# Kernel tuning notes

Measured on AMD Instinct MI355X. Metric: run time of the kernel, lower is better.

Reference implementation:

```python
import jax, jax.numpy as jnp
import numpy as np
from math import sqrt

B = 128        # graphs
P = 256        # nodes per graph
N = B * P      # total nodes
E = 524288     # edges (avg degree 16)
S = 32         # seed queries per graph
DQ = DK = DV = 128
H = 4          # heads


def setup_inputs() -> dict:
    key = jax.random.key(0)
    ks = jax.random.split(key, 10)
    Q = jax.random.normal(ks[0], (B, S, DQ), dtype=jnp.float32)
    x = jax.random.normal(ks[1], (N, DK), dtype=jnp.float32)
    # edges constrained within each graph block of P nodes
    src = jax.random.randint(ks[2], (E,), 0, N)
    dst = (src // P) * P + jax.random.randint(ks[3], (E,), 0, P)
    edge_index = jnp.stack([src, dst]).astype(jnp.int64)
    batch = (jnp.arange(N) // P).astype(jnp.int64)
    s = 1.0 / sqrt(DV)
    Wq = jax.random.normal(ks[4], (DQ, DV), dtype=jnp.float32) * s
    Wk = jax.random.normal(ks[5], (DK, DV), dtype=jnp.float32) * s
    Wv = jax.random.normal(ks[6], (DK, DV), dtype=jnp.float32) * s
    Wo = jax.random.normal(ks[7], (DV, DV), dtype=jnp.float32) * s
    z = jnp.zeros((DV,), jnp.float32)
    o = jnp.ones((DV,), jnp.float32)
    return {"Q": Q, "x": x, "edge_index": edge_index, "batch": batch,
            "Wq": Wq, "bq": z, "Wk": Wk, "bk": z, "Wv": Wv, "bv": z,
            "Wo": Wo, "bo": z, "g0": o, "b0": z, "g1": o, "b1": z}


def _gcn(x, edge_index, W, b):
    # PyG GCNConv: self-loops + symmetric deg^-1/2 normalization, then scatter-add
    xw = x @ W                                   # [N, DV]
    row, col = edge_index[0], edge_index[1]
    deg = jnp.zeros((N,), xw.dtype).at[col].add(1.0) + 1.0  # +1 for self-loop
    dinv = jax.lax.rsqrt(deg)
    coef = dinv[row] * dinv[col]                 # [E]
    out = jnp.zeros_like(xw).at[col].add(xw[row] * coef[:, None])
    out = out + xw * (dinv * dinv)[:, None]      # self-loop messages
    return out + b


def _ln(x, g, b, eps=1e-5):
    mu = x.mean(-1, keepdims=True)
    var = ((x - mu) ** 2).mean(-1, keepdims=True)
    return (x - mu) * jax.lax.rsqrt(var + eps) * g + b


def reference(Q, x, edge_index, batch, Wq, bq, Wk, bk, Wv, bv, Wo, bo, g0, b0, g1, b1):
    dh = DV // H
    Qp = Q @ Wq + bq                             # [B, S, DV]
    K = _gcn(x, edge_index, Wk, bk)              # [N, DV]
    V = _gcn(x, edge_index, Wv, bv)
    # to_dense_batch: equal-size graphs -> static reshape; mask all valid
    Kd = K.reshape(B, P, DV)
    Vd = V.reshape(B, P, DV)
    mask = jnp.ones((B, P), Qp.dtype)
    mask_add = (1.0 - mask) * -1e9               # [B, P]
    # split heads on last dim (== torch split(dim=2) + cat(dim=0))
    Qh = Qp.reshape(B, S, H, dh)
    Kh = Kd.reshape(B, P, H, dh)
    Vh = Vd.reshape(B, P, H, dh)
    scores = jnp.einsum('bshd,bphd->bhsp', Qh, Kh) / sqrt(DV)
    A = jax.nn.softmax(scores + mask_add[:, None, None, :], axis=-1)
    Oh = Qh + jnp.einsum('bhsp,bphd->bshd', A, Vh)
    O = Oh.reshape(B, S, DV)
    O = _ln(O, g0, b0)
    O = O + jax.nn.relu(O @ Wo + bo)
    O = _ln(O, g1, b1)
    return O
```

## Files before the change

### kernel.cpp

```cpp
#include <hip/hip_runtime.h>

typedef unsigned int uint32;
typedef unsigned short ushort;
typedef __attribute__((ext_vector_type(8))) short short8;
typedef __attribute__((ext_vector_type(4))) float f32x4;

#define NNODES 32768
#define NGRAPH 128
#define PNODES 256
#define SQ 32
#define NEDGE 524288
#define DIM 128
#define NHEAD 4
#define MAXDEG 64

__device__ __forceinline__ float u2f(uint32 u){ union{uint32 i; float f;} c; c.i=u; return c.f; }
__device__ __forceinline__ uint32 f2bf(float f){
  union{float f; uint32 i;} c; c.f=f;
  return (c.i + 0x7FFFu + ((c.i>>16)&1u)) >> 16;
}
__device__ __forceinline__ uint32 pk2(float a, float b){ return f2bf(a) | (f2bf(b)<<16); }

__device__ __forceinline__ void swz_pair(int b, int& g, int& h){
  const int xcd = b & 7, j = b >> 3;
  g = xcd * 16 + (j >> 1);
  h = j & 1;
}

__global__ __launch_bounds__(256) void k_prep0(const float* __restrict__ Wk,
    const float* __restrict__ Wv, const float* __restrict__ Wq, const float* __restrict__ Wo,
    ushort* __restrict__ WTk, ushort* __restrict__ WTv, ushort* __restrict__ WTq,
    ushort* __restrict__ WTo, int4* __restrict__ zbase){
  const int bid = blockIdx.x;
  const int t = threadIdx.x;
  if (bid >= 4){
    int idx = (bid-4)*256 + t;
    if (idx < 8192) zbase[idx] = int4{0,0,0,0};
    return;
  }
  __shared__ __align__(16) float Ws2[128*132];
  const float* W = (bid==0) ? Wk : (bid==1) ? Wv : (bid==2) ? Wq : Wo;
  ushort* WT     = (bid==0) ? WTk : (bid==1) ? WTv : (bid==2) ? WTq : WTo;
  for (int idx = t; idx < 4096; idx += 256){
    int k = idx >> 5, c4 = idx & 31;
    *(float4*)&Ws2[k*132 + c4*4] = *(const float4*)&W[k*128 + c4*4];
  }
  __syncthreads();
  for (int idx = t; idx < 2048; idx += 256){
    int n = idx & 127, c8 = idx >> 7;
    uint4 p;
    p.x = pk2(Ws2[(c8*8+0)*132 + n], Ws2[(c8*8+1)*132 + n]);
    p.y = pk2(Ws2[(c8*8+2)*132 + n], Ws2[(c8*8+3)*132 + n]);
    p.z = pk2(Ws2[(c8*8+4)*132 + n], Ws2[(c8*8+5)*132 + n]);
    p.w = pk2(Ws2[(c8*8+6)*132 + n], Ws2[(c8*8+7)*132 + n]);
    *(uint4*)&WT[n*128 + c8*8] = p;
  }
}

__global__ void k_edges(const int* __restrict__ ei, int* __restrict__ deg,
                        ushort* __restrict__ ebuf){
  int e = blockIdx.x*256 + threadIdx.x;
  int s = ei[e];
  int d = ei[NEDGE + e];
  int i = atomicAdd(&deg[d], 1);
  if (i < MAXDEG) ebuf[(d << 6) + i] = (ushort)(s & 255);
}

#define APITCH 132
__global__ __launch_bounds__(512) void k_aggkv(
    const int* __restrict__ deg, const ushort* __restrict__ ebuf,
    const float* __restrict__ x,
    const ushort* __restrict__ WTk, const float* __restrict__ bk, ushort* __restrict__ Kb,
    const ushort* __restrict__ WTv, const float* __restrict__ bv, ushort* __restrict__ VbT)
{
  __shared__ __align__(16) char lds[138240];
  uint32* A    = (uint32*)lds;
  ushort* Au   = (ushort*)lds;
  ushort* xT   = (ushort*)(lds + 67584);
  ushort* xa_s = (ushort*)(lds + 67584);
  ushort* wtA  = (ushort*)(lds + 102400);
  ushort* wtB  = (ushort*)(lds + 0);
  ushort* KK   = (ushort*)(lds + 67584);
  ushort* VVt  = (ushort*)(lds + 102400);
  float*  dvs  = (float*)(lds + 137216);
  const int t = threadIdx.x;
  int g, half;
  swz_pair(blockIdx.x, g, half);
  const int base = g*PNODES;
  const int rbase = half*128;

  if (t < 256) dvs[t] = rsqrtf((float)(deg[base + t] + 1));
  {
    uint4* Az = (uint4*)A;
    for (int i = t; i < 4224; i += 512) Az[i] = uint4{0,0,0,0};
  }
  __syncthreads();
  if (t < 128){
    float dn = dvs[rbase + t];
    int src = rbase + t;
    uint32 nb = f2bf(dn*dn);
    A[t*APITCH + (src>>1)] = (src & 1) ? (nb<<16) : nb;
  }
  for (int idx = t; idx < 8192; idx += 512){
    int f = idx & 127, s4 = idx >> 7;
    const int r = base + s4*4;
    float v0 = x[(r+0)*DIM + f];
    float v1 = x[(r+1)*DIM + f];
    float v2 = x[(r+2)*DIM + f];
    float v3 = x[(r+3)*DIM + f];
    uint2 p; p.x = pk2(v0, v1); p.y = pk2(v2, v3);
    *(uint2*)&xT[f*264 + s4*4] = p;
  }
  __syncthreads();
  {
    const int r = t >> 2, sub = t & 3;
    const int n = base + rbase + r;
    const int dg = min(deg[n], MAXDEG);
    const float dn = dvs[rbase + r];
    const ushort* eb = ebuf + (n << 6);
    for (int i = 0; i < dg; ++i){
      const int srcl = eb[i];
      if (((srcl >> 1) & 3) != sub) continue;
      const float coef = dn * dvs[srcl];
      uint32* cell = &A[r*APITCH + (srcl>>1)];
      uint32 old = *cell;
      if (srcl & 1){
        float cur = u2f(old & 0xffff0000u);
        *cell = (old & 0xffffu) | (f2bf(cur + coef) << 16);
      } else {
        float cur = u2f(old << 16);
        *cell = (old & 0xffff0000u) | f2bf(cur + coef);
      }
    }
  }
  __syncthreads();
  const int lane = t & 63, w = t >> 6;
  const int r16 = lane & 15, kg = lane >> 4;
  f32x4 acc[8];
  #pragma unroll
  for (int j = 0; j < 8; ++j) acc[j] = (f32x4){0.f,0.f,0.f,0.f};
  #pragma unroll
  for (int kc = 0; kc < 8; ++kc){
    const short8 a = *(const short8*)&Au[(w*16 + r16)*264 + kc*32 + kg*8];
    #pragma unroll
    for (int ct = 0; ct < 8; ++ct){
      const short8 b = *(const short8*)&xT[(ct*16 + r16)*264 + kc*32 + kg*8];
      acc[ct] = __builtin_amdgcn_mfma_f32_16x16x32_bf16(a, b, acc[ct], 0, 0, 0);
    }
  }
  __syncthreads();
  #pragma unroll
  for (int ct = 0; ct < 8; ++ct)
    #pragma unroll
    for (int q = 0; q < 4; ++q)
      xa_s[(w*16 + kg*4 + q)*136 + ct*16 + r16] = (ushort)f2bf(acc[ct][q]);
  for (int idx = t; idx < 2048; idx += 512){
    int n = idx >> 4, c8 = idx & 15;
    *(uint4*)&wtA[n*136 + c8*8] = *(const uint4*)&WTk[n*128 + c8*8];
    *(uint4*)&wtB[n*136 + c8*8] = *(const uint4*)&WTv[n*128 + c8*8];
  }
  __syncthreads();
  f32x4 k0[8], v0[8];
  #pragma unroll
  for (int j = 0; j < 8; ++j){ k0[j] = (f32x4){0.f,0.f,0.f,0.f}; v0[j] = (f32x4){0.f,0.f,0.f,0.f}; }
  #pragma unroll
  for (int kc = 0; kc < 4; ++kc){
    const short8 a = *(const short8*)&xa_s[(w*16 + r16)*136 + kc*32 + kg*8];
    #pragma unroll
    for (int ct = 0; ct < 8; ++ct){
      const short8 b0 = *(const short8*)&wtA[(ct*16 + r16)*136 + kc*32 + kg*8];
      const short8 b1 = *(const short8*)&wtB[(ct*16 + r16)*136 + kc*32 + kg*8];
      k0[ct] = __builtin_amdgcn_mfma_f32_16x16x32_bf16(a, b0, k0[ct], 0, 0, 0);
      v0[ct] = __builtin_amdgcn_mfma_f32_16x16x32_bf16(a, b1, v0[ct], 0, 0, 0);
    }
  }
  __syncthreads();
  #pragma unroll
  for (int ct = 0; ct < 8; ++ct){
    const int col = ct*16 + r16;
    const float bkc = bk[col], bvc = bv[col];
    #pragma unroll
    for (int q = 0; q < 4; ++q){
      const int r = w*16 + kg*4 + q;
      KK[r*136 + col]  = (ushort)f2bf(k0[ct][q] + bkc);
      VVt[col*136 + r] = (ushort)f2bf(v0[ct][q] + bvc);
    }
  }
  __syncthreads();
  for (int idx = t; idx < 2048; idx += 512){
    int r = idx >> 4, c8 = idx & 15;
    *(uint4*)&Kb[(base + rbase + r)*DIM + c8*8] = *(const uint4*)&KK[r*136 + c8*8];
  }
  for (int idx = t; idx < 2048; idx += 512){
    int d = idx >> 4, c8 = idx & 15;
    *(uint4*)&VbT[(g*128 + d)*PNODES + rbase + c8*8] = *(const uint4*)&VVt[d*136 + c8*8];
  }
}

__global__ __launch_bounds__(512) void k_attnepi(
    const float* __restrict__ Qin, const ushort* __restrict__ WTq,
    const float* __restrict__ bq,
    const ushort* __restrict__ Kb, const ushort* __restrict__ VbT,
    const ushort* __restrict__ WoT, const float* __restrict__ bo,
    const float* __restrict__ g0, const float* __restrict__ b0,
    const float* __restrict__ g1, const float* __restrict__ b1,
    float* __restrict__ out)
{
  __shared__ __align__(16) char lds[151040];
  ushort* KbS = (ushort*)lds;
  ushort* VT  = (ushort*)lds;
  ushort* R2  = (ushort*)(lds + 69632);
  float*  S   = (float*)(lds + 104448);
  float*  Zf  = (float*)(lds + 104448);
  ushort* Pb  = (ushort*)(lds + 121344);
  float*  Yf  = (float*)(lds + 121344);
  float*  Ob  = (float*)(lds + 129792);
  float*  Qres= (float*)(lds + 138240);
  ushort* Qb  = (ushort*)(lds + 146688);

  const int t = threadIdx.x;
  const int w = t >> 6, lane = t & 63;
  const int r16 = lane & 15, kg = lane >> 4;
  int g, qh;
  swz_pair(blockIdx.x, g, qh);
  const int qr0 = g*SQ + qh*16;

  for (int idx = t; idx < 4096; idx += 512){
    int r = idx >> 4, c8 = idx & 15;
    *(uint4*)&KbS[r*136 + c8*8] = *(const uint4*)&Kb[(g*256 + r)*128 + c8*8];
  }
  for (int idx = t; idx < 2048; idx += 512){
    int n = idx >> 4, c8 = idx & 15;
    *(uint4*)&R2[n*136 + c8*8] = *(const uint4*)&WTq[n*128 + c8*8];
  }
  short8 qin[4];
  #pragma unroll
  for (int kc = 0; kc < 4; ++kc){
    const float4 f0 = *(const float4*)&Qin[(qr0 + r16)*128 + kc*32 + kg*8];
    const float4 f1 = *(const float4*)&Qin[(qr0 + r16)*128 + kc*32 + kg*8 + 4];
    union { short8 s; uint32 u[4]; } c;
    c.u[0] = pk2(f0.x, f0.y); c.u[1] = pk2(f0.z, f0.w);
    c.u[2] = pk2(f1.x, f1.y); c.u[3] = pk2(f1.z, f1.w);
    qin[kc] = c.s;
  }
  __syncthreads();

  {
    f32x4 qa = (f32x4){0.f,0.f,0.f,0.f};
    #pragma unroll
    for (int kc = 0; kc < 4; ++kc){
      const short8 bf = *(const short8*)&R2[(w*16 + r16)*136 + kc*32 + kg*8];
      qa = __builtin_amdgcn_mfma_f32_16x16x32_bf16(qin[kc], bf, qa, 0, 0, 0);
    }
    #pragma unroll
    for (int q = 0; q < 4; ++q){
      const int row = kg*4 + q, col = w*16 + r16;
      const float v = qa[q] + bq[col];
      Qres[row*132 + col] = v;
      Qb[row*136 + col] = (ushort)f2bf(v);
    }
  }
  __syncthreads();

  {
    short8 qf[4];
    #pragma unroll
    for (int kc = 0; kc < 4; ++kc)
      qf[kc] = *(const short8*)&Qb[r16*136 + kc*32 + kg*8];
    f32x4 sa[2];
    sa[0] = (f32x4){0.f,0.f,0.f,0.f}; sa[1] = (f32x4){0.f,0.f,0.f,0.f};
    #pragma unroll
    for (int kc = 0; kc < 4; ++kc){
      #pragma unroll
      for (int nt = 0; nt < 2; ++nt){
        const short8 bf = *(const short8*)&KbS[((w*2+nt)*16 + r16)*136 + kc*32 + kg*8];
        sa[nt] = __builtin_amdgcn_mfma_f32_16x16x32_bf16(qf[kc], bf, sa[nt], 0, 0, 0);
      }
    }
    #pragma unroll
    for (int nt = 0; nt < 2; ++nt)
      #pragma unroll
      for (int q = 0; q < 4; ++q)
        S[(kg*4+q)*264 + (w*2+nt)*16 + r16] = sa[nt][q] * 0.08838834764831845f;
  }
  __syncthreads();

  {
    const int row = t >> 5, j = t & 31;
    float vals[8];
    float m = -1e30f;
    #pragma unroll
    for (int u = 0; u < 8; ++u){
      vals[u] = S[row*264 + j + 32*u];
      m = fmaxf(m, vals[u]);
    }
    m = fmaxf(m, __shfl_xor(m, 1));
    m = fmaxf(m, __shfl_xor(m, 2));
    m = fmaxf(m, __shfl_xor(m, 4));
    m = fmaxf(m, __shfl_xor(m, 8));
    m = fmaxf(m, __shfl_xor(m, 16));
    float sum = 0.f;
    #pragma unroll
    for (int u = 0; u < 8; ++u){
      vals[u] = __expf(vals[u] - m);
      sum += vals[u];
    }
    sum += __shfl_xor(sum, 1);
    sum += __shfl_xor(sum, 2);
    sum += __shfl_xor(sum, 4);
    sum += __shfl_xor(sum, 8);
    sum += __shfl_xor(sum, 16);
    float inv = 1.f / sum;
    #pragma unroll
    for (int u = 0; u < 8; ++u)
      Pb[row*264 + j + 32*u] = (ushort)f2bf(vals[u] * inv);
  }
  for (int idx = t; idx < 4096; idx += 512){
    int d = idx >> 5, c8 = idx & 31;
    *(uint4*)&VT[d*264 + c8*8] = *(const uint4*)&VbT[(g*128 + d)*PNODES + c8*8];
  }
  __syncthreads();

  {
    f32x4 oa = (f32x4){0.f,0.f,0.f,0.f};
    #pragma unroll
    for (int kc = 0; kc < 8; ++kc){
      const short8 pa = *(const short8*)&Pb[r16*264 + kc*32 + kg*8];
      const short8 vb = *(const short8*)&VT[(w*16 + r16)*264 + kc*32 + kg*8];
      oa = __builtin_amdgcn_mfma_f32_16x16x32_bf16(pa, vb, oa, 0, 0, 0);
    }
    #pragma unroll
    for (int q = 0; q < 4; ++q){
      const int row = kg*4 + q, col = w*16 + r16;
      Ob[row*132 + col] = oa[q] + Qres[row*132 + col];
    }
  }
  __syncthreads();

  #pragma unroll
  for (int rr = 0; rr < 2; ++rr){
    const int row = w*2 + rr;
    float x0 = Ob[row*132 + 2*lane], x1 = Ob[row*132 + 2*lane + 1];
    float s = x0 + x1;
    s += __shfl_xor(s,1); s += __shfl_xor(s,2); s += __shfl_xor(s,4);
    s += __shfl_xor(s,8); s += __shfl_xor(s,16); s += __shfl_xor(s,32);
    float mu = s * 0.0078125f;
    float d0 = x0 - mu, d1 = x1 - mu;
    float vv = d0*d0 + d1*d1;
    vv += __shfl_xor(vv,1); vv += __shfl_xor(vv,2); vv += __shfl_xor(vv,4);
    vv += __shfl_xor(vv,8); vv += __shfl_xor(vv,16); vv += __shfl_xor(vv,32);
    float rs = rsqrtf(vv*0.0078125f + 1e-5f);
    const float2 gv = *(const float2*)&g0[2*lane];
    const float2 bv = *(const float2*)&b0[2*lane];
    float y0 = d0*rs*gv.x + bv.x;
    float y1 = d1*rs*gv.y + bv.y;
    Yf[row*132 + 2*lane] = y0; Yf[row*132 + 2*lane + 1] = y1;
    *(uint32*)&Qb[row*136 + 2*lane] = pk2(y0, y1);
  }
  for (int idx = t; idx < 2048; idx += 512){
    int n = idx >> 4, c8 = idx & 15;
    *(uint4*)&R2[n*136 + c8*8] = *(const uint4*)&WoT[n*128 + c8*8];
  }
  __syncthreads();

  {
    f32x4 fa = (f32x4){0.f,0.f,0.f,0.f};
    #pragma unroll
    for (int kc = 0; kc < 4; ++kc){
      const short8 ya = *(const short8*)&Qb[r16*136 + kc*32 + kg*8];
      const short8 wb = *(const short8*)&R2[(w*16 + r16)*136 + kc*32 + kg*8];
      fa = __builtin_amdgcn_mfma_f32_16x16x32_bf16(ya, wb, fa, 0, 0, 0);
    }
    #pragma unroll
    for (int q = 0; q < 4; ++q){
      const int row = kg*4 + q, col = w*16 + r16;
      Zf[row*132 + col] = Yf[row*132 + col] + fmaxf(fa[q] + bo[col], 0.f);
    }
  }
  __syncthreads();

  #pragma unroll
  for (int rr = 0; rr < 2; ++rr){
    const int row = w*2 + rr;
    float z0 = Zf[row*132 + 2*lane], z1 = Zf[row*132 + 2*lane + 1];
    float s = z0 + z1;
    s += __shfl_xor(s,1); s += __shfl_xor(s,2); s += __shfl_xor(s,4);
    s += __shfl_xor(s,8); s += __shfl_xor(s,16); s += __shfl_xor(s,32);
    float mu = s * 0.0078125f;
    float d0 = z0 - mu, d1 = z1 - mu;
    float vv = d0*d0 + d1*d1;
    vv += __shfl_xor(vv,1); vv += __shfl_xor(vv,2); vv += __shfl_xor(vv,4);
    vv += __shfl_xor(vv,8); vv += __shfl_xor(vv,16); vv += __shfl_xor(vv,32);
    float rs = rsqrtf(vv*0.0078125f + 1e-5f);
    const float2 g1v = *(const float2*)&g1[2*lane];
    const float2 b1v = *(const float2*)&b1[2*lane];
    float2 o;
    o.x = d0*rs*g1v.x + b1v.x;
    o.y = d1*rs*g1v.y + b1v.y;
    *(float2*)&out[(qr0 + row)*128 + 2*lane] = o;
  }
}

extern "C" void kernel_launch(void* const* d_in, const int* in_sizes, int n_in,
                              void* d_out, int out_size, void* d_ws, size_t ws_size,
                              hipStream_t stream){
  const float* Q   = (const float*)d_in[0];
  const float* x   = (const float*)d_in[1];
  const int*   ei  = (const int*)d_in[2];
  const float* Wq  = (const float*)d_in[4];
  const float* bq  = (const float*)d_in[5];
  const float* Wk  = (const float*)d_in[6];
  const float* bk  = (const float*)d_in[7];
  const float* Wv  = (const float*)d_in[8];
  const float* bv  = (const float*)d_in[9];
  const float* Wo  = (const float*)d_in[10];
  const float* bo  = (const float*)d_in[11];
  const float* g0  = (const float*)d_in[12];
  const float* b0  = (const float*)d_in[13];
  const float* g1  = (const float*)d_in[14];
  const float* b1  = (const float*)d_in[15];

  char* ws = (char*)d_ws;
  ushort* Kb   = (ushort*)(ws);
  ushort* VbT  = (ushort*)(ws + 8388608);
  ushort* WTk  = (ushort*)(ws + 16777216);
  ushort* WTv  = (ushort*)(ws + 16809984);
  ushort* WTq  = (ushort*)(ws + 16842752);
  ushort* WTo  = (ushort*)(ws + 16875520);
  int*    deg  = (int*)(ws + 16908288);
  ushort* ebuf = (ushort*)(ws + 17039360);

  k_prep0<<<36, 256, 0, stream>>>(Wk, Wv, Wq, Wo, WTk, WTv, WTq, WTo, (int4*)deg);
  k_edges<<<NEDGE/256, 256, 0, stream>>>(ei, deg, ebuf);
  k_aggkv<<<NGRAPH*2, 512, 0, stream>>>(deg, ebuf, x, WTk, bk, Kb, WTv, bv, VbT);
  k_attnepi<<<NGRAPH*2, 512, 0, stream>>>(Q, WTq, bq, Kb, VbT, WTo, bo, g0, b0, g1, b1, (float*)d_out);
}
```

Measured before the change: 70.53 us.

## Fuse all four kernels into one cooperative megakernel with grid syncs

Merges the weight prep/zeroing, edge bucketing, K/V aggregation and attention-epilogue kernels into a single cooperative kernel of 256 blocks. Grid-wide barriers replace the kernel boundaries between stages. The aim is to remove launch overhead and inter-kernel gaps across four launches. In exchange it adds grid.sync costs, runs the edge scatter on only 256 blocks instead of 2048, and forces one block per CU at full LDS size.

```diff
diff --git a/kernel.cpp b/kernel.cpp
--- a/kernel.cpp
+++ b/kernel.cpp
@@ -1,4 +1,5 @@
 #include <hip/hip_runtime.h>
+#include <hip/hip_cooperative_groups.h>
 
 typedef unsigned int uint32;
 typedef unsigned short ushort;
@@ -27,411 +28,402 @@
   h = j & 1;
 }
 
-__global__ __launch_bounds__(256) void k_prep0(const float* __restrict__ Wk,
-    const float* __restrict__ Wv, const float* __restrict__ Wq, const float* __restrict__ Wo,
-    ushort* __restrict__ WTk, ushort* __restrict__ WTv, ushort* __restrict__ WTq,
-    ushort* __restrict__ WTo, int4* __restrict__ zbase){
-  const int bid = blockIdx.x;
-  const int t = threadIdx.x;
-  if (bid >= 4){
-    int idx = (bid-4)*256 + t;
-    if (idx < 8192) zbase[idx] = int4{0,0,0,0};
-    return;
-  }
-  __shared__ __align__(16) float Ws2[128*132];
-  const float* W = (bid==0) ? Wk : (bid==1) ? Wv : (bid==2) ? Wq : Wo;
-  ushort* WT     = (bid==0) ? WTk : (bid==1) ? WTv : (bid==2) ? WTq : WTo;
-  for (int idx = t; idx < 4096; idx += 256){
-    int k = idx >> 5, c4 = idx & 31;
-    *(float4*)&Ws2[k*132 + c4*4] = *(const float4*)&W[k*128 + c4*4];
-  }
-  __syncthreads();
-  for (int idx = t; idx < 2048; idx += 256){
-    int n = idx & 127, c8 = idx >> 7;
-    uint4 p;
-    p.x = pk2(Ws2[(c8*8+0)*132 + n], Ws2[(c8*8+1)*132 + n]);
-    p.y = pk2(Ws2[(c8*8+2)*132 + n], Ws2[(c8*8+3)*132 + n]);
-    p.z = pk2(Ws2[(c8*8+4)*132 + n], Ws2[(c8*8+5)*132 + n]);
-    p.w = pk2(Ws2[(c8*8+6)*132 + n], Ws2[(c8*8+7)*132 + n]);
-    *(uint4*)&WT[n*128 + c8*8] = p;
-  }
-}
-
-__global__ void k_edges(const int* __restrict__ ei, int* __restrict__ deg,
-                        ushort* __restrict__ ebuf){
-  int e = blockIdx.x*256 + threadIdx.x;
-  int s = ei[e];
-  int d = ei[NEDGE + e];
-  int i = atomicAdd(&deg[d], 1);
-  if (i < MAXDEG) ebuf[(d << 6) + i] = (ushort)(s & 255);
-}
+struct MegaArgs {
+  const float* Q; const float* x; const int* ei;
+  const float *Wq, *bq, *Wk, *bk, *Wv, *bv, *Wo, *bo, *g0, *b0, *g1, *b1;
+  float* out;
+  ushort *WTk, *WTv, *WTq, *WTo;
+  int* deg; ushort* ebuf; ushort* Kb; ushort* VbT;
+};
 
 #define APITCH 132
-__global__ __launch_bounds__(512) void k_aggkv(
-    const int* __restrict__ deg, const ushort* __restrict__ ebuf,
-    const float* __restrict__ x,
-    const ushort* __restrict__ WTk, const float* __restrict__ bk, ushort* __restrict__ Kb,
-    const ushort* __restrict__ WTv, const float* __restrict__ bv, ushort* __restrict__ VbT)
+
+__global__ __launch_bounds__(512, 1) void k_mega(MegaArgs a)
 {
-  __shared__ __align__(16) char lds[138240];
-  uint32* A    = (uint32*)lds;
-  ushort* Au   = (ushort*)lds;
-  ushort* xT   = (ushort*)(lds + 67584);
-  ushort* xa_s = (ushort*)(lds + 67584);
-  ushort* wtA  = (ushort*)(lds + 102400);
-  ushort* wtB  = (ushort*)(lds + 0);
-  ushort* KK   = (ushort*)(lds + 67584);
-  ushort* VVt  = (ushort*)(lds + 102400);
-  float*  dvs  = (float*)(lds + 137216);
-  const int t = threadIdx.x;
-  int g, half;
-  swz_pair(blockIdx.x, g, half);
-  const int base = g*PNODES;
-  const int rbase = half*128;
-
-  if (t < 256) dvs[t] = rsqrtf((float)(deg[base + t] + 1));
-  {
-    uint4* Az = (uint4*)A;
-    for (int i = t; i < 4224; i += 512) Az[i] = uint4{0,0,0,0};
-  }
-  __syncthreads();
-  if (t < 128){
-    float dn = dvs[rbase + t];
-    int src = rbase + t;
-    uint32 nb = f2bf(dn*dn);
-    A[t*APITCH + (src>>1)] = (src & 1) ? (nb<<16) : nb;
-  }
-  for (int idx = t; idx < 8192; idx += 512){
-    int f = idx & 127, s4 = idx >> 7;
-    const int r = base + s4*4;
-    float v0 = x[(r+0)*DIM + f];
-    float v1 = x[(r+1)*DIM + f];
-    float v2 = x[(r+2)*DIM + f];
-    float v3 = x[(r+3)*DIM + f];
-    uint2 p; p.x = pk2(v0, v1); p.y = pk2(v2, v3);
-    *(uint2*)&xT[f*264 + s4*4] = p;
-  }
-  __syncthreads();
-  {
-    const int r = t >> 2, sub = t & 3;
-    const int n = base + rbase + r;
-    const int dg = min(deg[n], MAXDEG);
-    const float dn = dvs[rbase + r];
-    const ushort* eb = ebuf + (n << 6);
-    for (int i = 0; i < dg; ++i){
-      const int srcl = eb[i];
-      if (((srcl >> 1) & 3) != sub) continue;
-      const float coef = dn * dvs[srcl];
-      uint32* cell = &A[r*APITCH + (srcl>>1)];
-      uint32 old = *cell;
-      if (srcl & 1){
-        float cur = u2f(old & 0xffff0000u);
-        *cell = (old & 0xffffu) | (f2bf(cur + coef) << 16);
-      } else {
-        float cur = u2f(old << 16);
-        *cell = (old & 0xffff0000u) | f2bf(cur + coef);
-      }
-    }
-  }
-  __syncthreads();
+  __shared__ __align__(16) char lds[151040];
+  cooperative_groups::grid_group grid = cooperative_groups::this_grid();
+  const int t = threadIdx.x, bid = blockIdx.x;
+  const int tid = bid*512 + t;
   const int lane = t & 63, w = t >> 6;
   const int r16 = lane & 15, kg = lane >> 4;
-  f32x4 acc[8];
+
+  if (tid < 8192) ((int4*)a.deg)[tid] = int4{0,0,0,0};
+  grid.sync();
+
   #pragma unroll
-  for (int j = 0; j < 8; ++j) acc[j] = (f32x4){0.f,0.f,0.f,0.f};
-  #pragma unroll
-  for (int kc = 0; kc < 8; ++kc){
-    const short8 a = *(const short8*)&Au[(w*16 + r16)*264 + kc*32 + kg*8];
+  for (int j = 0; j < 4; ++j){
+    const int e = tid + j*131072;
+    const int s = a.ei[e];
+    const int d = a.ei[NEDGE + e];
+    const int i = atomicAdd(&a.deg[d], 1);
+    if (i < MAXDEG) a.ebuf[(d << 6) + i] = (ushort)(s & 255);
+  }
+  if (bid < 4){
+    float* Ws2 = (float*)lds;
+    const float* W = (bid==0) ? a.Wk : (bid==1) ? a.Wv : (bid==2) ? a.Wq : a.Wo;
+    ushort* WT     = (bid==0) ? a.WTk : (bid==1) ? a.WTv : (bid==2) ? a.WTq : a.WTo;
+    for (int idx = t; idx < 4096; idx += 512){
+      int k = idx >> 5, c4 = idx & 31;
+      *(float4*)&Ws2[k*132 + c4*4] = *(const float4*)&W[k*128 + c4*4];
+    }
+    __syncthreads();
+    for (int idx = t; idx < 2048; idx += 512){
+      int n = idx & 127, c8 = idx >> 7;
+      uint4 p;
+      p.x = pk2(Ws2[(c8*8+0)*132 + n], Ws2[(c8*8+1)*132 + n]);
+      p.y = pk2(Ws2[(c8*8+2)*132 + n], Ws2[(c8*8+3)*132 + n]);
+      p.z = pk2(Ws2[(c8*8+4)*132 + n], Ws2[(c8*8+5)*132 + n]);
+      p.w = pk2(Ws2[(c8*8+6)*132 + n], Ws2[(c8*8+7)*132 + n]);
+      *(uint4*)&WT[n*128 + c8*8] = p;
+    }
+  }
+  grid.sync();
+
+  {
+    uint32* A    = (uint32*)lds;
+    ushort* Au   = (ushort*)lds;
+    ushort* xT   = (ushort*)(lds + 67584);
+    ushort* xa_s = (ushort*)(lds + 67584);
+    ushort* wtA  = (ushort*)(lds + 102400);
+    ushort* wtB  = (ushort*)(lds + 0);
+    ushort* KK   = (ushort*)(lds + 67584);
+    ushort* VVt  = (ushort*)(lds + 102400);
+    float*  dvs  = (float*)(lds + 137216);
+    int g, half;
+    swz_pair(bid, g, half);
+    const int base = g*PNODES;
+    const int rbase = half*128;
+
+    if (t < 256) dvs[t] = rsqrtf((float)(a.deg[base + t] + 1));
+    {
+      uint4* Az = (uint4*)A;
+      for (int i = t; i < 4224; i += 512) Az[i] = uint4{0,0,0,0};
+    }
+    __syncthreads();
+    if (t < 128){
+      float dn = dvs[rbase + t];
+      int src = rbase + t;
+      uint32 nb = f2bf(dn*dn);
+      A[t*APITCH + (src>>1)] = (src & 1) ? (nb<<16) : nb;
+    }
+    for (int idx = t; idx < 8192; idx += 512){
+      int f = idx & 127, s4 = idx >> 7;
+      const int r = base + s4*4;
+      float v0 = a.x[(r+0)*DIM + f];
+      float v1 = a.x[(r+1)*DIM + f];
+      float v2 = a.x[(r+2)*DIM + f];
+      float v3 = a.x[(r+3)*DIM + f];
+      uint2 p; p.x = pk2(v0, v1); p.y = pk2(v2, v3);
+      *(uint2*)&xT[f*264 + s4*4] = p;
+    }
+    __syncthreads();
+    {
+      const int r = t >> 2, sub = t & 3;
+      const int n = base + rbase + r;
+      const int dg = min(a.deg[n], MAXDEG);
+      const float dn = dvs[rbase + r];
+      const ushort* eb = a.ebuf + (n << 6);
+      for (int i = 0; i < dg; ++i){
+        const int srcl = eb[i];
+        if (((srcl >> 1) & 3) != sub) continue;
+        const float coef = dn * dvs[srcl];
+        uint32* cell = &A[r*APITCH + (srcl>>1)];
+        uint32 old = *cell;
+        if (srcl & 1){
+          float cur = u2f(old & 0xffff0000u);
+          *cell = (old & 0xffffu) | (f2bf(cur + coef) << 16);
+        } else {
+          float cur = u2f(old << 16);
+          *cell = (old & 0xffff0000u) | f2bf(cur + coef);
+        }
+      }
+    }
+    __syncthreads();
+    f32x4 acc[8];
+    #pragma unroll
+    for (int j = 0; j < 8; ++j) acc[j] = (f32x4){0.f,0.f,0.f,0.f};
+    #pragma unroll
+    for (int kc = 0; kc < 8; ++kc){
+      const short8 av = *(const short8*)&Au[(w*16 + r16)*264 + kc*32 + kg*8];
+      #pragma unroll
+      for (int ct = 0; ct < 8; ++ct){
+        const short8 b = *(const short8*)&xT[(ct*16 + r16)*264 + kc*32 + kg*8];
+        acc[ct] = __builtin_amdgcn_mfma_f32_16x16x32_bf16(av, b, acc[ct], 0, 0, 0);
+      }
+    }
+    __syncthreads();
+    #pragma unroll
+    for (int ct = 0; ct < 8; ++ct)
+      #pragma unroll
+      for (int q = 0; q < 4; ++q)
+        xa_s[(w*16 + kg*4 + q)*136 + ct*16 + r16] = (ushort)f2bf(acc[ct][q]);
+    for (int idx = t; idx < 2048; idx += 512){
+      int n = idx >> 4, c8 = idx & 15;
+      *(uint4*)&wtA[n*136 + c8*8] = *(const uint4*)&a.WTk[n*128 + c8*8];
+      *(uint4*)&wtB[n*136 + c8*8] = *(const uint4*)&a.WTv[n*128 + c8*8];
+    }
+    __syncthreads();
+    f32x4 k0[8], v0[8];
+    #pragma unroll
+    for (int j = 0; j < 8; ++j){ k0[j] = (f32x4){0.f,0.f,0.f,0.f}; v0[j] = (f32x4){0.f,0.f,0.f,0.f}; }
+    #pragma unroll
+    for (int kc = 0; kc < 4; ++kc){
+      const short8 av = *(const short8*)&xa_s[(w*16 + r16)*136 + kc*32 + kg*8];
+      #pragma unroll
+      for (int ct = 0; ct < 8; ++ct){
+        const short8 b0 = *(const short8*)&wtA[(ct*16 + r16)*136 + kc*32 + kg*8];
+        const short8 b1 = *(const short8*)&wtB[(ct*16 + r16)*136 + kc*32 + kg*8];
+        k0[ct] = __builtin_amdgcn_mfma_f32_16x16x32_bf16(av, b0, k0[ct], 0, 0, 0);
+        v0[ct] = __builtin_amdgcn_mfma_f32_16x16x32_bf16(av, b1, v0[ct], 0, 0, 0);
+      }
+    }
+    __syncthreads();
     #pragma unroll
     for (int ct = 0; ct < 8; ++ct){
-      const short8 b = *(const short8*)&xT[(ct*16 + r16)*264 + kc*32 + kg*8];
-      acc[ct] = __builtin_amdgcn_mfma_f32_16x16x32_bf16(a, b, acc[ct], 0, 0, 0);
+      const int col = ct*16 + r16;
+      const float bkc = a.bk[col], bvc = a.bv[col];
+      #pragma unroll
+      for (int q = 0; q < 4; ++q){
+        const int r = w*16 + kg*4 + q;
+        KK[r*136 + col]  = (ushort)f2bf(k0[ct][q] + bkc);
+        VVt[col*136 + r] = (ushort)f2bf(v0[ct][q] + bvc);
+      }
+    }
+    __syncthreads();
+    for (int idx = t; idx < 2048; idx += 512){
+      int r = idx >> 4, c8 = idx & 15;
+      *(uint4*)&a.Kb[(base + rbase + r)*DIM + c8*8] = *(const uint4*)&KK[r*136 + c8*8];
+    }
+    for (int idx = t; idx < 2048; idx += 512){
+      int d = idx >> 4, c8 = idx & 15;
+      *(uint4*)&a.VbT[(g*128 + d)*PNODES + rbase + c8*8] = *(const uint4*)&VVt[d*136 + c8*8];
     }
   }
-  __syncthreads();
-  #pragma unroll
-  for (int ct = 0; ct < 8; ++ct)
-    #pragma unroll
-    for (int q = 0; q < 4; ++q)
-      xa_s[(w*16 + kg*4 + q)*136 + ct*16 + r16] = (ushort)f2bf(acc[ct][q]);
-  for (int idx = t; idx < 2048; idx += 512){
-    int n = idx >> 4, c8 = idx & 15;
-    *(uint4*)&wtA[n*136 + c8*8] = *(const uint4*)&WTk[n*128 + c8*8];
-    *(uint4*)&wtB[n*136 + c8*8] = *(const uint4*)&WTv[n*128 + c8*8];
-  }
-  __syncthreads();
-  f32x4 k0[8], v0[8];
-  #pragma unroll
-  for (int j = 0; j < 8; ++j){ k0[j] = (f32x4){0.f,0.f,0.f,0.f}; v0[j] = (f32x4){0.f,0.f,0.f,0.f}; }
-  #pragma unroll
-  for (int kc = 0; kc < 4; ++kc){
-    const short8 a = *(const short8*)&xa_s[(w*16 + r16)*136 + kc*32 + kg*8];
-    #pragma unroll
-    for (int ct = 0; ct < 8; ++ct){
-      const short8 b0 = *(const short8*)&wtA[(ct*16 + r16)*136 + kc*32 + kg*8];
-      const short8 b1 = *(const short8*)&wtB[(ct*16 + r16)*136 + kc*32 + kg*8];
-      k0[ct] = __builtin_amdgcn_mfma_f32_16x16x32_bf16(a, b0, k0[ct], 0, 0, 0);
-      v0[ct] = __builtin_amdgcn_mfma_f32_16x16x32_bf16(a, b1, v0[ct], 0, 0, 0);
-    }
-  }
-  __syncthreads();
-  #pragma unroll
-  for (int ct = 0; ct < 8; ++ct){
-    const int col = ct*16 + r16;
-    const float bkc = bk[col], bvc = bv[col];
-    #pragma unroll
-    for (int q = 0; q < 4; ++q){
-      const int r = w*16 + kg*4 + q;
-      KK[r*136 + col]  = (ushort)f2bf(k0[ct][q] + bkc);
-      VVt[col*136 + r] = (ushort)f2bf(v0[ct][q] + bvc);
-    }
-  }
-  __syncthreads();
-  for (int idx = t; idx < 2048; idx += 512){
-    int r = idx >> 4, c8 = idx & 15;
-    *(uint4*)&Kb[(base + rbase + r)*DIM + c8*8] = *(const uint4*)&KK[r*136 + c8*8];
-  }
-  for (int idx = t; idx < 2048; idx += 512){
-    int d = idx >> 4, c8 = idx & 15;
-    *(uint4*)&VbT[(g*128 + d)*PNODES + rbase + c8*8] = *(const uint4*)&VVt[d*136 + c8*8];
-  }
-}
-
-__global__ __launch_bounds__(512) void k_attnepi(
-    const float* __restrict__ Qin, const ushort* __restrict__ WTq,
-    const float* __restrict__ bq,
-    const ushort* __restrict__ Kb, const ushort* __restrict__ VbT,
-    const ushort* __restrict__ WoT, const float* __restrict__ bo,
-    const float* __restrict__ g0, const float* __restrict__ b0,
-    const float* __restrict__ g1, const float* __restrict__ b1,
-    float* __restrict__ out)
-{
-  __shared__ __align__(16) char lds[151040];
-  ushort* KbS = (ushort*)lds;
-  ushort* VT  = (ushort*)lds;
-  ushort* R2  = (ushort*)(lds + 69632);
-  float*  S   = (float*)(lds + 104448);
-  float*  Zf  = (float*)(lds + 104448);
-  ushort* Pb  = (ushort*)(lds + 121344);
-  float*  Yf  = (float*)(lds + 121344);
-  float*  Ob  = (float*)(lds + 129792);
-  float*  Qres= (float*)(lds + 138240);
-  ushort* Qb  = (ushort*)(lds + 146688);
-
-  const int t = threadIdx.x;
-  const int w = t >> 6, lane = t & 63;
-  const int r16 = lane & 15, kg = lane >> 4;
-  int g, qh;
-  swz_pair(blockIdx.x, g, qh);
-  const int qr0 = g*SQ + qh*16;
-
-  for (int idx = t; idx < 4096; idx += 512){
-    int r = idx >> 4, c8 = idx & 15;
-    *(uint4*)&KbS[r*136 + c8*8] = *(const uint4*)&Kb[(g*256 + r)*128 + c8*8];
-  }
-  for (int idx = t; idx < 2048; idx += 512){
-    int n = idx >> 4, c8 = idx & 15;
-    *(uint4*)&R2[n*136 + c8*8] = *(const uint4*)&WTq[n*128 + c8*8];
-  }
-  short8 qin[4];
-  #pragma unroll
-  for (int kc = 0; kc < 4; ++kc){
-    const float4 f0 = *(const float4*)&Qin[(qr0 + r16)*128 + kc*32 + kg*8];
-    const float4 f1 = *(const float4*)&Qin[(qr0 + r16)*128 + kc*32 + kg*8 + 4];
-    union { short8 s; uint32 u[4]; } c;
-    c.u[0] = pk2(f0.x, f0.y); c.u[1] = pk2(f0.z, f0.w);
-    c.u[2] = pk2(f1.x, f1.y); c.u[3] = pk2(f1.z, f1.w);
-    qin[kc] = c.s;
-  }
-  __syncthreads();
+  grid.sync();
 
   {
-    f32x4 qa = (f32x4){0.f,0.f,0.f,0.f};
+    ushort* KbS = (ushort*)lds;
+    ushort* VT  = (ushort*)lds;
+    ushort* R2  = (ushort*)(lds + 69632);
+    float*  S   = (float*)(lds + 104448);
+    float*  Zf  = (float*)(lds + 104448);
+    ushort* Pb  = (ushort*)(lds + 121344);
+    float*  Yf  = (float*)(lds + 121344);
+    float*  Ob  = (float*)(lds + 129792);
+    float*  Qres= (float*)(lds + 138240);
+    ushort* Qb  = (ushort*)(lds + 146688);
+    int g, qh;
+    swz_pair(bid, g, qh);
+    const int qr0 = g*SQ + qh*16;
+
+    for (int idx = t; idx < 4096; idx += 512){
+      int r = idx >> 4, c8 = idx & 15;
+      *(uint4*)&KbS[r*136 + c8*8] = *(const uint4*)&a.Kb[(g*256 + r)*128 + c8*8];
+    }
+    for (int idx = t; idx < 2048; idx += 512){
+      int n = idx >> 4, c8 = idx & 15;
+      *(uint4*)&R2[n*136 + c8*8] = *(const uint4*)&a.WTq[n*128 + c8*8];
+    }
+    short8 qin[4];
     #pragma unroll
     for (int kc = 0; kc < 4; ++kc){
-      const short8 bf = *(const short8*)&R2[(w*16 + r16)*136 + kc*32 + kg*8];
-      qa = __builtin_amdgcn_mfma_f32_16x16x32_bf16(qin[kc], bf, qa, 0, 0, 0);
-    }
-    #pragma unroll
-    for (int q = 0; q < 4; ++q){
-      const int row = kg*4 + q, col = w*16 + r16;
-      const float v = qa[q] + bq[col];
-      Qres[row*132 + col] = v;
-      Qb[row*136 + col] = (ushort)f2bf(v);
-    }
-  }
-  __syncthreads();
-
-  {
-    short8 qf[4];
-    #pragma unroll
-    for (int kc = 0; kc < 4; ++kc)
-      qf[kc] = *(const short8*)&Qb[r16*136 + kc*32 + kg*8];
-    f32x4 sa[2];
-    sa[0] = (f32x4){0.f,0.f,0.f,0.f}; sa[1] = (f32x4){0.f,0.f,0.f,0.f};
-    #pragma unroll
-    for (int kc = 0; kc < 4; ++kc){
-      #pragma unroll
-      for (int nt = 0; nt < 2; ++nt){
-        const short8 bf = *(const short8*)&KbS[((w*2+nt)*16 + r16)*136 + kc*32 + kg*8];
-        sa[nt] = __builtin_amdgcn_mfma_f32_16x16x32_bf16(qf[kc], bf, sa[nt], 0, 0, 0);
-      }
-    }
-    #pragma unroll
-    for (int nt = 0; nt < 2; ++nt)
-      #pragma unroll
-      for (int q = 0; q < 4; ++q)
-        S[(kg*4+q)*264 + (w*2+nt)*16 + r16] = sa[nt][q] * 0.08838834764831845f;
-  }
-  __syncthreads();
-
-  {
-    const int row = t >> 5, j = t & 31;
-    float vals[8];
-    float m = -1e30f;
-    #pragma unroll
-    for (int u = 0; u < 8; ++u){
-      vals[u] = S[row*264 + j + 32*u];
-      m = fmaxf(m, vals[u]);
-    }
-    m = fmaxf(m, __shfl_xor(m, 1));
-    m = fmaxf(m, __shfl_xor(m, 2));
-    m = fmaxf(m, __shfl_xor(m, 4));
-    m = fmaxf(m, __shfl_xor(m, 8));
-    m = fmaxf(m, __shfl_xor(m, 16));
-    float sum = 0.f;
-    #pragma unroll
-    for (int u = 0; u < 8; ++u){
-      vals[u] = __expf(vals[u] - m);
-      sum += vals[u];
-    }
-    sum += __shfl_xor(sum, 1);
-    sum += __shfl_xor(sum, 2);
-    sum += __shfl_xor(sum, 4);
-    sum += __shfl_xor(sum, 8);
-    sum += __shfl_xor(sum, 16);
-    float inv = 1.f / sum;
-    #pragma unroll
-    for (int u = 0; u < 8; ++u)
-      Pb[row*264 + j + 32*u] = (ushort)f2bf(vals[u] * inv);
-  }
-  for (int idx = t; idx < 4096; idx += 512){
-    int d = idx >> 5, c8 = idx & 31;
-    *(uint4*)&VT[d*264 + c8*8] = *(const uint4*)&VbT[(g*128 + d)*PNODES + c8*8];
-  }
-  __syncthreads();
-
-  {
-    f32x4 oa = (f32x4){0.f,0.f,0.f,0.f};
-    #pragma unroll
-    for (int kc = 0; kc < 8; ++kc){
-      const short8 pa = *(const short8*)&Pb[r16*264 + kc*32 + kg*8];
-      const short8 vb = *(const short8*)&VT[(w*16 + r16)*264 + kc*32 + kg*8];
-      oa = __builtin_amdgcn_mfma_f32_16x16x32_bf16(pa, vb, oa, 0, 0, 0);
-    }
-    #pragma unroll
-    for (int q = 0; q < 4; ++q){
-      const int row = kg*4 + q, col = w*16 + r16;
-      Ob[row*132 + col] = oa[q] + Qres[row*132 + col];
-    }
-  }
-  __syncthreads();
-
-  #pragma unroll
-  for (int rr = 0; rr < 2; ++rr){
-    const int row = w*2 + rr;
-    float x0 = Ob[row*132 + 2*lane], x1 = Ob[row*132 + 2*lane + 1];
-    float s = x0 + x1;
-    s += __shfl_xor(s,1); s += __shfl_xor(s,2); s += __shfl_xor(s,4);
-    s += __shfl_xor(s,8); s += __shfl_xor(s,16); s += __shfl_xor(s,32);
-    float mu = s * 0.0078125f;
-    float d0 = x0 - mu, d1 = x1 - mu;
-    float vv = d0*d0 + d1*d1;
-    vv += __shfl_xor(vv,1); vv += __shfl_xor(vv,2); vv += __shfl_xor(vv,4);
-    vv += __shfl_xor(vv,8); vv += __shfl_xor(vv,16); vv += __shfl_xor(vv,32);
-    float rs = rsqrtf(vv*0.0078125f + 1e-5f);
-    const float2 gv = *(const float2*)&g0[2*lane];
-    const float2 bv = *(const float2*)&b0[2*lane];
-    float y0 = d0*rs*gv.x + bv.x;
-    float y1 = d1*rs*gv.y + bv.y;
-    Yf[row*132 + 2*lane] = y0; Yf[row*132 + 2*lane + 1] = y1;
-    *(uint32*)&Qb[row*136 + 2*lane] = pk2(y0, y1);
-  }
-  for (int idx = t; idx < 2048; idx += 512){
-    int n = idx >> 4, c8 = idx & 15;
-    *(uint4*)&R2[n*136 + c8*8] = *(const uint4*)&WoT[n*128 + c8*8];
-  }
-  __syncthreads();
-
-  {
-    f32x4 fa = (f32x4){0.f,0.f,0.f,0.f};
-    #pragma unroll
-    for (int kc = 0; kc < 4; ++kc){
-      const short8 ya = *(const short8*)&Qb[r16*136 + kc*32 + kg*8];
-      const short8 wb = *(const short8*)&R2[(w*16 + r16)*136 + kc*32 + kg*8];
-      fa = __builtin_amdgcn_mfma_f32_16x16x32_bf16(ya, wb, fa, 0, 0, 0);
-    }
-    #pragma unroll
-    for (int q = 0; q < 4; ++q){
-      const int row = kg*4 + q, col = w*16 + r16;
-      Zf[row*132 + col] = Yf[row*132 + col] + fmaxf(fa[q] + bo[col], 0.f);
-    }
-  }
-  __syncthreads();
-
-  #pragma unroll
-  for (int rr = 0; rr < 2; ++rr){
-    const int row = w*2 + rr;
-    float z0 = Zf[row*132 + 2*lane], z1 = Zf[row*132 + 2*lane + 1];
-    float s = z0 + z1;
-    s += __shfl_xor(s,1); s += __shfl_xor(s,2); s += __shfl_xor(s,4);
-    s += __shfl_xor(s,8); s += __shfl_xor(s,16); s += __shfl_xor(s,32);
-    float mu = s * 0.0078125f;
-    float d0 = z0 - mu, d1 = z1 - mu;
-    float vv = d0*d0 + d1*d1;
-    vv += __shfl_xor(vv,1); vv += __shfl_xor(vv,2); vv += __shfl_xor(vv,4);
-    vv += __shfl_xor(vv,8); vv += __shfl_xor(vv,16); vv += __shfl_xor(vv,32);
-    float rs = rsqrtf(vv*0.0078125f + 1e-5f);
-    const float2 g1v = *(const float2*)&g1[2*lane];
-    const float2 b1v = *(const float2*)&b1[2*lane];
-    float2 o;
-    o.x = d0*rs*g1v.x + b1v.x;
-    o.y = d1*rs*g1v.y + b1v.y;
-    *(float2*)&out[(qr0 + row)*128 + 2*lane] = o;
+      const float4 f0 = *(const float4*)&a.Q[(qr0 + r16)*128 + kc*32 + kg*8];
+      const float4 f1 = *(const float4*)&a.Q[(qr0 + r16)*128 + kc*32 + kg*8 + 4];
+      union { short8 s; uint32 u[4]; } c;
+      c.u[0] = pk2(f0.x, f0.y); c.u[1] = pk2(f0.z, f0.w);
+      c.u[2] = pk2(f1.x, f1.y); c.u[3] = pk2(f1.z, f1.w);
+      qin[kc] = c.s;
+    }
+    __syncthreads();
+
+    {
+      f32x4 qa = (f32x4){0.f,0.f,0.f,0.f};
+      #pragma unroll
+      for (int kc = 0; kc < 4; ++kc){
+        const short8 bf = *(const short8*)&R2[(w*16 + r16)*136 + kc*32 + kg*8];
+        qa = __builtin_amdgcn_mfma_f32_16x16x32_bf16(qin[kc], bf, qa, 0, 0, 0);
+      }
+      #pragma unroll
+      for (int q = 0; q < 4; ++q){
+        const int row = kg*4 + q, col = w*16 + r16;
+        const float v = qa[q] + a.bq[col];
+        Qres[row*132 + col] = v;
+        Qb[row*136 + col] = (ushort)f2bf(v);
+      }
+    }
+    __syncthreads();
+
+    {
+      short8 qf[4];
+      #pragma unroll
+      for (int kc = 0; kc < 4; ++kc)
+        qf[kc] = *(const short8*)&Qb[r16*136 + kc*32 + kg*8];
+      f32x4 sa[2];
+      sa[0] = (f32x4){0.f,0.f,0.f,0.f}; sa[1] = (f32x4){0.f,0.f,0.f,0.f};
+      #pragma unroll
+      for (int kc = 0; kc < 4; ++kc){
+        #pragma unroll
+        for (int nt = 0; nt < 2; ++nt){
+          const short8 bf = *(const short8*)&KbS[((w*2+nt)*16 + r16)*136 + kc*32 + kg*8];
+          sa[nt] = __builtin_amdgcn_mfma_f32_16x16x32_bf16(qf[kc], bf, sa[nt], 0, 0, 0);
+        }
+      }
+      #pragma unroll
+      for (int nt = 0; nt < 2; ++nt)
+        #pragma unroll
+        for (int q = 0; q < 4; ++q)
+          S[(kg*4+q)*264 + (w*2+nt)*16 + r16] = sa[nt][q] * 0.08838834764831845f;
+    }
+    __syncthreads();
+
+    {
+      const int row = t >> 5, j = t & 31;
+      float vals[8];
+      float m = -1e30f;
+      #pragma unroll
+      for (int u = 0; u < 8; ++u){
+        vals[u] = S[row*264 + j + 32*u];
+        m = fmaxf(m, vals[u]);
+      }
+      m = fmaxf(m, __shfl_xor(m, 1));
+      m = fmaxf(m, __shfl_xor(m, 2));
+      m = fmaxf(m, __shfl_xor(m, 4));
+      m = fmaxf(m, __shfl_xor(m, 8));
+      m = fmaxf(m, __shfl_xor(m, 16));
+      float sum = 0.f;
+      #pragma unroll
+      for (int u = 0; u < 8; ++u){
+        vals[u] = __expf(vals[u] - m);
+        sum += vals[u];
+      }
+      sum += __shfl_xor(sum, 1);
+      sum += __shfl_xor(sum, 2);
+      sum += __shfl_xor(sum, 4);
+      sum += __shfl_xor(sum, 8);
+      sum += __shfl_xor(sum, 16);
+      float inv = 1.f / sum;
+      #pragma unroll
+      for (int u = 0; u < 8; ++u)
+        Pb[row*264 + j + 32*u] = (ushort)f2bf(vals[u] * inv);
+    }
+    for (int idx = t; idx < 4096; idx += 512){
+      int d = idx >> 5, c8 = idx & 31;
+      *(uint4*)&VT[d*264 + c8*8] = *(const uint4*)&a.VbT[(g*128 + d)*PNODES + c8*8];
+    }
+    __syncthreads();
+
+    {
+      f32x4 oa = (f32x4){0.f,0.f,0.f,0.f};
+      #pragma unroll
+      for (int kc = 0; kc < 8; ++kc){
+        const short8 pa = *(const short8*)&Pb[r16*264 + kc*32 + kg*8];
+        const short8 vb = *(const short8*)&VT[(w*16 + r16)*264 + kc*32 + kg*8];
+        oa = __builtin_amdgcn_mfma_f32_16x16x32_bf16(pa, vb, oa, 0, 0, 0);
+      }
+      #pragma unroll
+      for (int q = 0; q < 4; ++q){
+        const int row = kg*4 + q, col = w*16 + r16;
+        Ob[row*132 + col] = oa[q] + Qres[row*132 + col];
+      }
+    }
+    __syncthreads();
+
+    #pragma unroll
+    for (int rr = 0; rr < 2; ++rr){
+      const int row = w*2 + rr;
+      float x0 = Ob[row*132 + 2*lane], x1 = Ob[row*132 + 2*lane + 1];
+      float s = x0 + x1;
+      s += __shfl_xor(s,1); s += __shfl_xor(s,2); s += __shfl_xor(s,4);
+      s += __shfl_xor(s,8); s += __shfl_xor(s,16); s += __shfl_xor(s,32);
+      float mu = s * 0.0078125f;
+      float d0 = x0 - mu, d1 = x1 - mu;
+      float vv = d0*d0 + d1*d1;
+      vv += __shfl_xor(vv,1); vv += __shfl_xor(vv,2); vv += __shfl_xor(vv,4);
+      vv += __shfl_xor(vv,8); vv += __shfl_xor(vv,16); vv += __shfl_xor(vv,32);
+      float rs = rsqrtf(vv*0.0078125f + 1e-5f);
+      const float2 gv = *(const float2*)&a.g0[2*lane];
+      const float2 bv = *(const float2*)&a.b0[2*lane];
+      float y0 = d0*rs*gv.x + bv.x;
+      float y1 = d1*rs*gv.y + bv.y;
+      Yf[row*132 + 2*lane] = y0; Yf[row*132 + 2*lane + 1] = y1;
+      *(uint32*)&Qb[row*136 + 2*lane] = pk2(y0, y1);
+    }
+    for (int idx = t; idx < 2048; idx += 512){
+      int n = idx >> 4, c8 = idx & 15;
+      *(uint4*)&R2[n*136 + c8*8] = *(const uint4*)&a.WTo[n*128 + c8*8];
+    }
+    __syncthreads();
+
+    {
+      f32x4 fa = (f32x4){0.f,0.f,0.f,0.f};
+      #pragma unroll
+      for (int kc = 0; kc < 4; ++kc){
+        const short8 ya = *(const short8*)&Qb[r16*136 + kc*32 + kg*8];
+        const short8 wb = *(const short8*)&R2[(w*16 + r16)*136 + kc*32 + kg*8];
+        fa = __builtin_amdgcn_mfma_f32_16x16x32_bf16(ya, wb, fa, 0, 0, 0);
+      }
+      #pragma unroll
+      for (int q = 0; q < 4; ++q){
+        const int row = kg*4 + q, col = w*16 + r16;
+        Zf[row*132 + col] = Yf[row*132 + col] + fmaxf(fa[q] + a.bo[col], 0.f);
+      }
+    }
+    __syncthreads();
+
+    #pragma unroll
+    for (int rr = 0; rr < 2; ++rr){
+      const int row = w*2 + rr;
+      float z0 = Zf[row*132 + 2*lane], z1 = Zf[row*132 + 2*lane + 1];
+      float s = z0 + z1;
+      s += __shfl_xor(s,1); s += __shfl_xor(s,2); s += __shfl_xor(s,4);
+      s += __shfl_xor(s,8); s += __shfl_xor(s,16); s += __shfl_xor(s,32);
+      float mu = s * 0.0078125f;
+      float d0 = z0 - mu, d1 = z1 - mu;
+      float vv = d0*d0 + d1*d1;
+      vv += __shfl_xor(vv,1); vv += __shfl_xor(vv,2); vv += __shfl_xor(vv,4);
+      vv += __shfl_xor(vv,8); vv += __shfl_xor(vv,16); vv += __shfl_xor(vv,32);
+      float rs = rsqrtf(vv*0.0078125f + 1e-5f);
+      const float2 g1v = *(const float2*)&a.g1[2*lane];
+      const float2 b1v = *(const float2*)&a.b1[2*lane];
+      float2 o;
+      o.x = d0*rs*g1v.x + b1v.x;
+      o.y = d1*rs*g1v.y + b1v.y;
+      *(float2*)&a.out[(qr0 + row)*128 + 2*lane] = o;
+    }
   }
 }
 
 extern "C" void kernel_launch(void* const* d_in, const int* in_sizes, int n_in,
                               void* d_out, int out_size, void* d_ws, size_t ws_size,
                               hipStream_t stream){
-  const float* Q   = (const float*)d_in[0];
-  const float* x   = (const float*)d_in[1];
-  const int*   ei  = (const int*)d_in[2];
-  const float* Wq  = (const float*)d_in[4];
-  const float* bq  = (const float*)d_in[5];
-  const float* Wk  = (const float*)d_in[6];
-  const float* bk  = (const float*)d_in[7];
-  const float* Wv  = (const float*)d_in[8];
-  const float* bv  = (const float*)d_in[9];
-  const float* Wo  = (const float*)d_in[10];
-  const float* bo  = (const float*)d_in[11];
-  const float* g0  = (const float*)d_in[12];
-  const float* b0  = (const float*)d_in[13];
-  const float* g1  = (const float*)d_in[14];
-  const float* b1  = (const float*)d_in[15];
-
   char* ws = (char*)d_ws;
-  ushort* Kb   = (ushort*)(ws);
-  ushort* VbT  = (ushort*)(ws + 8388608);
-  ushort* WTk  = (ushort*)(ws + 16777216);
-  ushort* WTv  = (ushort*)(ws + 16809984);
-  ushort* WTq  = (ushort*)(ws + 16842752);
-  ushort* WTo  = (ushort*)(ws + 16875520);
-  int*    deg  = (int*)(ws + 16908288);
-  ushort* ebuf = (ushort*)(ws + 17039360);
-
-  k_prep0<<<36, 256, 0, stream>>>(Wk, Wv, Wq, Wo, WTk, WTv, WTq, WTo, (int4*)deg);
-  k_edges<<<NEDGE/256, 256, 0, stream>>>(ei, deg, ebuf);
-  k_aggkv<<<NGRAPH*2, 512, 0, stream>>>(deg, ebuf, x, WTk, bk, Kb, WTv, bv, VbT);
-  k_attnepi<<<NGRAPH*2, 512, 0, stream>>>(Q, WTq, bq, Kb, VbT, WTo, bo, g0, b0, g1, b1, (float*)d_out);
+  MegaArgs ha;
+  ha.Q   = (const float*)d_in[0];
+  ha.x   = (const float*)d_in[1];
+  ha.ei  = (const int*)d_in[2];
+  ha.Wq  = (const float*)d_in[4];
+  ha.bq  = (const float*)d_in[5];
+  ha.Wk  = (const float*)d_in[6];
+  ha.bk  = (const float*)d_in[7];
+  ha.Wv  = (const float*)d_in[8];
+  ha.bv  = (const float*)d_in[9];
+  ha.Wo  = (const float*)d_in[10];
+  ha.bo  = (const float*)d_in[11];
+  ha.g0  = (const float*)d_in[12];
+  ha.b0  = (const float*)d_in[13];
+  ha.g1  = (const float*)d_in[14];
+  ha.b1  = (const float*)d_in[15];
+  ha.out = (float*)d_out;
+  ha.Kb  = (ushort*)(ws);
+  ha.VbT = (ushort*)(ws + 8388608);
+  ha.WTk = (ushort*)(ws + 16777216);
+  ha.WTv = (ushort*)(ws + 16809984);
+  ha.WTq = (ushort*)(ws + 16842752);
+  ha.WTo = (ushort*)(ws + 16875520);
+  ha.deg = (int*)(ws + 16908288);
+  ha.ebuf= (ushort*)(ws + 17039360);
+
+  void* kargs[] = { &ha };
+  hipLaunchCooperativeKernel((const void*)k_mega, dim3(256), dim3(512),
+                             kargs, 0, stream);
 }
```

After: 172.4 us. 144% more time.
